# Kernel tuning notes

Measured on AMD Instinct MI355X. Metric: run time of the kernel, lower is better.

## Reference

```python
import jax, jax.numpy as jnp
import numpy as np

N_NODES = 100000


def setup_inputs() -> dict:
    key = jax.random.key(0)
    k1, k2, k3 = jax.random.split(key, 3)
    x = jax.random.normal(k1, (N_NODES, 128), dtype=jnp.float32)
    # Flattened hyperedge membership: src_idx = member node ids, dst_idx = target
    # node id of the owning hyperedge (repeated once per member).
    src_idx = jax.random.randint(k2, (2000000,), 0, N_NODES, dtype=jnp.int64)
    dst_idx = jax.random.randint(k3, (2000000,), 0, N_NODES, dtype=jnp.int64)
    return {"x": x, "src_idx": src_idx, "dst_idx": dst_idx}


def reference(x, src_idx, dst_idx):
    # Gather member features, aggregate per target node, add residual.
    # (The torch identity-stack weight matmul is exactly a per-hyperedge sum,
    #  which the flattened scatter_add reproduces.)
    x_j = x[src_idx]                                        # [E_total, d]
    agg = jax.ops.segment_sum(x_j, dst_idx, num_segments=x.shape[0])  # [N, d]
    return x + agg
```

## Files before the change

kernel.cpp:

```cpp
#include <hip/hip_runtime.h>


constexpr int DIM = 128;
constexpr int BSHIFT = 7;
constexpr int GNODES = 1 << BSHIFT;
constexpr int MAXB = 1024;
constexpr int CE = 8192;
constexpr int CAP_MAX = 3072;
constexpr int QCAP = 1536;

__device__ inline unsigned short f2bf(float f) {
    unsigned u = __float_as_uint(f);
    u = (u + 0x7FFFu + ((u >> 16) & 1u)) >> 16;
    return (unsigned short)u;
}
__device__ inline float bf2f(unsigned short h) {
    return __uint_as_float((unsigned)h << 16);
}

__global__ void hgnn_convert_partition(const float4* __restrict__ x4,
                                       ushort4* __restrict__ xh4, int n4,
                                       const int* __restrict__ src,
                                       const int* __restrict__ dst,
                                       int* __restrict__ cursor,
                                       int* __restrict__ arena, int cap,
                                       int* __restrict__ spillCnt,
                                       int2* __restrict__ spill, int spillCap,
                                       int nedges, int nbk, int nPart) {
    __shared__ int h[MAXB];
    __shared__ int lb[MAXB];
    const int tid = threadIdx.x;

    if ((int)blockIdx.x < nPart) {
        int c0 = blockIdx.x * CE;
        int c1 = min(c0 + CE, nedges);
        for (int i = tid; i < nbk; i += blockDim.x) h[i] = 0;
        __syncthreads();
        for (int i = c0 + tid; i < c1; i += blockDim.x)
            atomicAdd(&h[dst[i] >> BSHIFT], 1);
        __syncthreads();
        for (int i = tid; i < nbk; i += blockDim.x)
            lb[i] = h[i] ? atomicAdd(&cursor[i], h[i]) : 0;
        __syncthreads();
        for (int i = c0 + tid; i < c1; i += blockDim.x) {
            int s = src[i];
            int d = dst[i];
            int bk = d >> BSHIFT;
            int pos = atomicAdd(&lb[bk], 1);
            if (pos < cap) {
                arena[(size_t)bk * cap + pos] = s | ((d & (GNODES - 1)) << 17);
            } else {
                int sp = atomicAdd(spillCnt, 1);
                if (sp < spillCap) spill[sp] = make_int2(s, d);
            }
        }
    } else {
        int bid = blockIdx.x - nPart;
        int nconv = gridDim.x - nPart;
        int i = bid * blockDim.x + tid;
        int stride = nconv * blockDim.x;
        for (int k = i; k < n4; k += stride) {
            float4 v = x4[k];
            ushort4 o;
            o.x = f2bf(v.x); o.y = f2bf(v.y);
            o.z = f2bf(v.z); o.w = f2bf(v.w);
            xh4[k] = o;
        }
        if (bid == 0 && tid < DIM / 4) {
            ushort4 z; z.x = 0; z.y = 0; z.z = 0; z.w = 0;
            xh4[n4 + tid] = z;
        }
    }
}

__global__ void hgnn_aggregate_sorted(const float4* __restrict__ x4,
                                      const ushort4* __restrict__ xh4,
                                      const int* __restrict__ arena, int cap,
                                      const int* __restrict__ cursor,
                                      float4* __restrict__ out4, int nnodes,
                                      int* __restrict__ spillCnt,
                                      int2* __restrict__ spill, int spillCap) {
    __shared__ int qsorted[QCAP];
    __shared__ int hoff[33];
    __shared__ int hcur[32];

    const int b = blockIdx.x >> 2;
    const int q = blockIdx.x & 3;
    const int tid = threadIdx.x;
    const int wv = tid >> 6;
    const int lane = tid & 63;
    const int h = lane >> 5;
    const int c = lane & 31;
    const int ZROW = nnodes;

    int cnt = cursor[b];
    if (cnt > cap) cnt = cap;
    const int* ar = arena + (size_t)b * cap;

    if (tid < 32) hcur[tid] = 0;
    __syncthreads();
    for (int i = tid; i < cnt; i += blockDim.x) {
        int dl = ar[i] >> 17;
        if ((dl >> 5) == q) atomicAdd(&hcur[dl & 31], 1);
    }
    __syncthreads();

    int myc = (tid < 32) ? hcur[tid] : 0;
    if (tid < 32) hoff[tid + 1] = myc;
    if (tid == 0) hoff[0] = 0;
    __syncthreads();
    for (int off = 1; off < 32; off <<= 1) {
        int v = (tid < 32 && tid >= off) ? hoff[tid + 1 - off] : 0;
        __syncthreads();
        if (tid < 32) hoff[tid + 1] += v;
        __syncthreads();
    }
    if (tid < 32) hcur[tid] = hoff[tid];
    __syncthreads();

    for (int i = tid; i < cnt; i += blockDim.x) {
        int p = ar[i];
        int dl = p >> 17;
        if ((dl >> 5) == q) {
            int pos = atomicAdd(&hcur[dl & 31], 1);
            if (pos < QCAP) {
                qsorted[pos] = p;
            } else {
                int sp = atomicAdd(spillCnt, 1);
                if (sp < spillCap)
                    spill[sp] = make_int2(p & 0x1FFFF, (b << BSHIFT) + dl);
            }
        }
    }
    __syncthreads();

    const int nodeBase = (b << BSHIFT) + q * 32 + wv * 8;
    for (int r = 0; r < 8; ++r) {
        int node = nodeBase + r;
        if (node >= nnodes) break;
        int bin = node & 31;
        int s0 = hoff[bin];
        int m = hoff[bin + 1] - s0;
        if (m > QCAP - s0) m = QCAP - s0;

        float4 acc = make_float4(0.f, 0.f, 0.f, 0.f);
        for (int j = 0; j < m; j += 16) {
#pragma unroll
            for (int k = 0; k < 8; ++k) {
                int e = j + 2 * k + h;
                bool ok = e < m;
                int p = ok ? (qsorted[s0 + e] & 0x1FFFF) : ZROW;
                ushort4 v = xh4[(size_t)p * 32 + c];
                acc.x += bf2f(v.x);
                acc.y += bf2f(v.y);
                acc.z += bf2f(v.z);
                acc.w += bf2f(v.w);
            }
        }

        acc.x += __shfl_xor(acc.x, 32);
        acc.y += __shfl_xor(acc.y, 32);
        acc.z += __shfl_xor(acc.z, 32);
        acc.w += __shfl_xor(acc.w, 32);

        if (h == 0) {
            float4 xv = x4[(size_t)node * 32 + c];
            out4[(size_t)node * 32 + c] =
                make_float4(xv.x + acc.x, xv.y + acc.y, xv.z + acc.z, xv.w + acc.w);
        }
    }
}

__global__ void hgnn_spill_apply(const float4* __restrict__ x4,
                                 const int* __restrict__ spillCnt,
                                 const int2* __restrict__ spill,
                                 float* __restrict__ out, int spillCap) {
    int n = *spillCnt;
    if (n > spillCap) n = spillCap;
    int i = blockIdx.x * blockDim.x + threadIdx.x;
    int stride = gridDim.x * blockDim.x;
    for (int k = i; k < n * 32; k += stride) {
        int e = k >> 5;
        int cc = k & 31;
        int2 sd = spill[e];
        float4 v = x4[(size_t)sd.x * 32 + cc];
        float* o = out + (size_t)sd.y * DIM + cc * 4;
        atomicAdd(o + 0, v.x);
        atomicAdd(o + 1, v.y);
        atomicAdd(o + 2, v.z);
        atomicAdd(o + 3, v.w);
    }
}

static inline size_t align256(size_t v) { return (v + 255) & ~(size_t)255; }

extern "C" void kernel_launch(void* const* d_in, const int* in_sizes, int n_in,
                              void* d_out, int out_size, void* d_ws, size_t ws_size,
                              hipStream_t stream) {
    const float* x = (const float*)d_in[0];
    const int* src = (const int*)d_in[1];
    const int* dst = (const int*)d_in[2];
    float* out = (float*)d_out;

    const int E = in_sizes[1];
    const int N = in_sizes[0] / DIM;
    const int n4 = N * (DIM / 4);
    const int NBK = (N + GNODES - 1) >> BSHIFT;
    const int nPart = (E + CE - 1) / CE;

    char* w = (char*)d_ws;
    size_t curBytes = align256((size_t)(MAXB + 1) * sizeof(int));
    size_t xhBytes = align256((size_t)(N + 1) * DIM * 2);
    size_t fixedBytes = curBytes + xhBytes;
    size_t spillReserve = 256 * 1024;

    size_t avail = (ws_size > fixedBytes + spillReserve)
                       ? (ws_size - fixedBytes - spillReserve) : 0;
    int cap = (int)((avail / sizeof(int)) / (size_t)NBK);
    if (cap > CAP_MAX) cap = CAP_MAX;
    if (cap < 64) cap = 64;

    int* cursor = (int*)w;
    int* spillCnt = cursor + MAXB;
    ushort* xh = (ushort*)(w + curBytes);
    int* arena = (int*)(w + fixedBytes);
    size_t arenaBytes = align256((size_t)NBK * cap * sizeof(int));
    int2* spill = (int2*)(w + fixedBytes + arenaBytes);
    int spillCap = (int)((ws_size > fixedBytes + arenaBytes)
                             ? (ws_size - fixedBytes - arenaBytes) / sizeof(int2)
                             : 0);

    hipMemsetAsync(cursor, 0, (size_t)(MAXB + 1) * sizeof(int), stream);

    {
        int grid = nPart + 1792;
        hipLaunchKernelGGL(hgnn_convert_partition, dim3(grid), dim3(256), 0,
                           stream, (const float4*)x, (ushort4*)xh, n4,
                           src, dst, cursor, arena, cap,
                           spillCnt, spill, spillCap, E, NBK, nPart);
    }

    hipLaunchKernelGGL(hgnn_aggregate_sorted, dim3(NBK * 4), dim3(256), 0, stream,
                       (const float4*)x, (const ushort4*)xh, arena, cap,
                       cursor, (float4*)out, N, spillCnt, spill, spillCap);

    hipLaunchKernelGGL(hgnn_spill_apply, dim3(64), dim3(256), 0, stream,
                       (const float4*)x, spillCnt, spill, out, spillCap);
}
```

Measured before the change: 141.1 us.

## Switch gather cache to fp16 with half2 accumulation, dynamic conversion chunks, two-node interleave

```diff
diff --git a/kernel.cpp b/kernel.cpp
--- a/kernel.cpp
+++ b/kernel.cpp
@@ -1,4 +1,5 @@
 #include <hip/hip_runtime.h>
+#include <hip/hip_fp16.h>
 
 
 constexpr int DIM = 128;
@@ -8,27 +9,21 @@
 constexpr int CE = 8192;
 constexpr int CAP_MAX = 3072;
 constexpr int QCAP = 1536;
-
-__device__ inline unsigned short f2bf(float f) {
-    unsigned u = __float_as_uint(f);
-    u = (u + 0x7FFFu + ((u >> 16) & 1u)) >> 16;
-    return (unsigned short)u;
-}
-__device__ inline float bf2f(unsigned short h) {
-    return __uint_as_float((unsigned)h << 16);
-}
-
-__global__ void hgnn_convert_partition(const float4* __restrict__ x4,
-                                       ushort4* __restrict__ xh4, int n4,
-                                       const int* __restrict__ src,
-                                       const int* __restrict__ dst,
-                                       int* __restrict__ cursor,
-                                       int* __restrict__ arena, int cap,
-                                       int* __restrict__ spillCnt,
-                                       int2* __restrict__ spill, int spillCap,
-                                       int nedges, int nbk, int nPart) {
+constexpr int CONVCH = 8192;
+
+__global__ void hgnn_fused_prep(const float4* __restrict__ x4,
+                                ushort4* __restrict__ xh4, int n4,
+                                const int* __restrict__ src,
+                                const int* __restrict__ dst,
+                                int* __restrict__ cursor,
+                                int* __restrict__ arena, int cap,
+                                int* __restrict__ spillCnt,
+                                int2* __restrict__ spill, int spillCap,
+                                int* __restrict__ qctr, int nChunks,
+                                int nedges, int nbk, int nPart) {
     __shared__ int h[MAXB];
     __shared__ int lb[MAXB];
+    __shared__ int chunkS;
     const int tid = threadIdx.x;
 
     if ((int)blockIdx.x < nPart) {
@@ -54,32 +49,40 @@
                 if (sp < spillCap) spill[sp] = make_int2(s, d);
             }
         }
-    } else {
-        int bid = blockIdx.x - nPart;
-        int nconv = gridDim.x - nPart;
-        int i = bid * blockDim.x + tid;
-        int stride = nconv * blockDim.x;
-        for (int k = i; k < n4; k += stride) {
-            float4 v = x4[k];
-            ushort4 o;
-            o.x = f2bf(v.x); o.y = f2bf(v.y);
-            o.z = f2bf(v.z); o.w = f2bf(v.w);
-            xh4[k] = o;
-        }
-        if (bid == 0 && tid < DIM / 4) {
+    } else if ((int)blockIdx.x == nPart) {
+        if (tid < 32) {
             ushort4 z; z.x = 0; z.y = 0; z.z = 0; z.w = 0;
             xh4[n4 + tid] = z;
         }
     }
-}
-
-__global__ void hgnn_aggregate_sorted(const float4* __restrict__ x4,
-                                      const ushort4* __restrict__ xh4,
-                                      const int* __restrict__ arena, int cap,
-                                      const int* __restrict__ cursor,
-                                      float4* __restrict__ out4, int nnodes,
-                                      int* __restrict__ spillCnt,
-                                      int2* __restrict__ spill, int spillCap) {
+
+    for (;;) {
+        if (tid == 0) chunkS = atomicAdd(qctr, 1);
+        __syncthreads();
+        int chunk = chunkS;
+        __syncthreads();
+        if (chunk >= nChunks) break;
+        int i0 = chunk * CONVCH;
+        int i1 = min(i0 + CONVCH, n4);
+        for (int i = i0 + tid; i < i1; i += blockDim.x) {
+            float4 v = x4[i];
+            ushort4 o;
+            o.x = __half_as_ushort(__float2half_rn(v.x));
+            o.y = __half_as_ushort(__float2half_rn(v.y));
+            o.z = __half_as_ushort(__float2half_rn(v.z));
+            o.w = __half_as_ushort(__float2half_rn(v.w));
+            xh4[i] = o;
+        }
+    }
+}
+
+__global__ void hgnn_aggregate(const float4* __restrict__ x4,
+                               const uint2* __restrict__ xh,
+                               const int* __restrict__ arena, int cap,
+                               const int* __restrict__ cursor,
+                               float4* __restrict__ out4, int nnodes,
+                               int* __restrict__ spillCnt,
+                               int2* __restrict__ spill, int spillCap) {
     __shared__ int qsorted[QCAP];
     __shared__ int hoff[33];
     __shared__ int hcur[32];
@@ -135,38 +138,80 @@
     __syncthreads();
 
     const int nodeBase = (b << BSHIFT) + q * 32 + wv * 8;
-    for (int r = 0; r < 8; ++r) {
-        int node = nodeBase + r;
-        if (node >= nnodes) break;
-        int bin = node & 31;
-        int s0 = hoff[bin];
-        int m = hoff[bin + 1] - s0;
-        if (m > QCAP - s0) m = QCAP - s0;
-
-        float4 acc = make_float4(0.f, 0.f, 0.f, 0.f);
-        for (int j = 0; j < m; j += 16) {
+    const __half2 hz = __floats2half2_rn(0.f, 0.f);
+    for (int r = 0; r < 8; r += 2) {
+        int n0 = nodeBase + r;
+        if (n0 >= nnodes) break;
+        int n1 = n0 + 1;
+        bool has1 = n1 < nnodes;
+
+        int bin0 = wv * 8 + r;
+        int s0 = hoff[bin0];
+        int e0 = hoff[bin0 + 1];
+        int s1 = hoff[bin0 + 1];
+        int e1 = hoff[bin0 + 2];
+        if (s0 > QCAP) s0 = QCAP;
+        if (e0 > QCAP) e0 = QCAP;
+        if (s1 > QCAP) s1 = QCAP;
+        if (e1 > QCAP) e1 = QCAP;
+        int m0 = e0 - s0;
+        int m1 = has1 ? (e1 - s1) : 0;
+        int mm = max(m0, m1);
+
+        __half2 a0lo = hz, a0hi = hz, b0lo = hz, b0hi = hz;
+        __half2 a1lo = hz, a1hi = hz, b1lo = hz, b1hi = hz;
+
+        for (int j = 0; j < mm; j += 16) {
 #pragma unroll
             for (int k = 0; k < 8; ++k) {
                 int e = j + 2 * k + h;
-                bool ok = e < m;
-                int p = ok ? (qsorted[s0 + e] & 0x1FFFF) : ZROW;
-                ushort4 v = xh4[(size_t)p * 32 + c];
-                acc.x += bf2f(v.x);
-                acc.y += bf2f(v.y);
-                acc.z += bf2f(v.z);
-                acc.w += bf2f(v.w);
-            }
-        }
-
-        acc.x += __shfl_xor(acc.x, 32);
-        acc.y += __shfl_xor(acc.y, 32);
-        acc.z += __shfl_xor(acc.z, 32);
-        acc.w += __shfl_xor(acc.w, 32);
-
-        if (h == 0) {
-            float4 xv = x4[(size_t)node * 32 + c];
-            out4[(size_t)node * 32 + c] =
-                make_float4(xv.x + acc.x, xv.y + acc.y, xv.z + acc.z, xv.w + acc.w);
+                int p0 = (e < m0) ? (qsorted[s0 + e] & 0x1FFFF) : ZROW;
+                int p1 = (e < m1) ? (qsorted[s1 + e] & 0x1FFFF) : ZROW;
+                uint2 v0 = xh[(size_t)p0 * 32 + c];
+                uint2 v1 = xh[(size_t)p1 * 32 + c];
+                __half2 v0lo = *reinterpret_cast<const __half2*>(&v0.x);
+                __half2 v0hi = *reinterpret_cast<const __half2*>(&v0.y);
+                __half2 v1lo = *reinterpret_cast<const __half2*>(&v1.x);
+                __half2 v1hi = *reinterpret_cast<const __half2*>(&v1.y);
+                if (k & 1) {
+                    b0lo = __hadd2(b0lo, v0lo); b0hi = __hadd2(b0hi, v0hi);
+                    b1lo = __hadd2(b1lo, v1lo); b1hi = __hadd2(b1hi, v1hi);
+                } else {
+                    a0lo = __hadd2(a0lo, v0lo); a0hi = __hadd2(a0hi, v0hi);
+                    a1lo = __hadd2(a1lo, v1lo); a1hi = __hadd2(a1hi, v1hi);
+                }
+            }
+        }
+
+        {
+            __half2 slo = __hadd2(a0lo, b0lo);
+            __half2 shi = __hadd2(a0hi, b0hi);
+            float2 flo = __half22float2(slo);
+            float2 fhi = __half22float2(shi);
+            float ax = flo.x + __shfl_xor(flo.x, 32);
+            float ay = flo.y + __shfl_xor(flo.y, 32);
+            float az = fhi.x + __shfl_xor(fhi.x, 32);
+            float aw = fhi.y + __shfl_xor(fhi.y, 32);
+            if (h == 0) {
+                float4 xv = x4[(size_t)n0 * 32 + c];
+                out4[(size_t)n0 * 32 + c] =
+                    make_float4(xv.x + ax, xv.y + ay, xv.z + az, xv.w + aw);
+            }
+        }
+        if (has1) {
+            __half2 slo = __hadd2(a1lo, b1lo);
+            __half2 shi = __hadd2(a1hi, b1hi);
+            float2 flo = __half22float2(slo);
+            float2 fhi = __half22float2(shi);
+            float ax = flo.x + __shfl_xor(flo.x, 32);
+            float ay = flo.y + __shfl_xor(flo.y, 32);
+            float az = fhi.x + __shfl_xor(fhi.x, 32);
+            float aw = fhi.y + __shfl_xor(fhi.y, 32);
+            if (h == 0) {
+                float4 xv = x4[(size_t)n1 * 32 + c];
+                out4[(size_t)n1 * 32 + c] =
+                    make_float4(xv.x + ax, xv.y + ay, xv.z + az, xv.w + aw);
+            }
         }
     }
 }
@@ -207,9 +252,10 @@
     const int n4 = N * (DIM / 4);
     const int NBK = (N + GNODES - 1) >> BSHIFT;
     const int nPart = (E + CE - 1) / CE;
+    const int nChunks = (n4 + CONVCH - 1) / CONVCH;
 
     char* w = (char*)d_ws;
-    size_t curBytes = align256((size_t)(MAXB + 1) * sizeof(int));
+    size_t curBytes = align256((size_t)(MAXB + 2) * sizeof(int));
     size_t xhBytes = align256((size_t)(N + 1) * DIM * 2);
     size_t fixedBytes = curBytes + xhBytes;
     size_t spillReserve = 256 * 1024;
@@ -222,6 +268,7 @@
 
     int* cursor = (int*)w;
     int* spillCnt = cursor + MAXB;
+    int* qctr = cursor + MAXB + 1;
     ushort* xh = (ushort*)(w + curBytes);
     int* arena = (int*)(w + fixedBytes);
     size_t arenaBytes = align256((size_t)NBK * cap * sizeof(int));
@@ -230,18 +277,19 @@
                              ? (ws_size - fixedBytes - arenaBytes) / sizeof(int2)
                              : 0);
 
-    hipMemsetAsync(cursor, 0, (size_t)(MAXB + 1) * sizeof(int), stream);
+    (void)hipMemsetAsync(cursor, 0, (size_t)(MAXB + 2) * sizeof(int), stream);
 
     {
-        int grid = nPart + 1792;
-        hipLaunchKernelGGL(hgnn_convert_partition, dim3(grid), dim3(256), 0,
-                           stream, (const float4*)x, (ushort4*)xh, n4,
+        int grid = nPart + 1024;
+        hipLaunchKernelGGL(hgnn_fused_prep, dim3(grid), dim3(256), 0, stream,
+                           (const float4*)x, (ushort4*)xh, n4,
                            src, dst, cursor, arena, cap,
-                           spillCnt, spill, spillCap, E, NBK, nPart);
-    }
-
-    hipLaunchKernelGGL(hgnn_aggregate_sorted, dim3(NBK * 4), dim3(256), 0, stream,
-                       (const float4*)x, (const ushort4*)xh, arena, cap,
+                           spillCnt, spill, spillCap,
+                           qctr, nChunks, E, NBK, nPart);
+    }
+
+    hipLaunchKernelGGL(hgnn_aggregate, dim3(NBK * 4), dim3(256), 0, stream,
+                       (const float4*)x, (const uint2*)xh, arena, cap,
                        cursor, (float4*)out, N, spillCnt, spill, spillCap);
 
     hipLaunchKernelGGL(hgnn_spill_apply, dim3(64), dim3(256), 0, stream,
```

Result: slower. 147.6 us (+4.6%).
